# Kernel tuning notes

Hardware: AMD Instinct MI355X
Metric: run time of the kernel (lower is better)

Reference implementation:

```python
import jax, jax.numpy as jnp
import numpy as np

def setup_inputs() -> dict:
    key = jax.random.key(0)
    k1, k2 = jax.random.split(key)
    N, M, D = 4096, 4096, 1024
    set1 = jax.random.normal(k1, (N, D), dtype=jnp.float32)
    set2 = jax.random.normal(k2, (M, D), dtype=jnp.float32)
    return {"set1": set1, "set2": set2}

def _l2_dist(x, y):
    # mean over D of squared differences, computed via the expanded GEMM form
    D = x.shape[-1]
    x2 = jnp.sum(x * x, axis=-1)          # [N]
    y2 = jnp.sum(y * y, axis=-1)          # [M]
    xy = jnp.einsum('nd,md->nm', x, y)    # [N, M]
    return (x2[:, None] - 2.0 * xy + y2[None, :]) / D

def reference(set1, set2):
    dist = _l2_dist(set1, set2)                 # [N, M]
    t1 = jnp.mean(jnp.min(dist, axis=1))        # nearest set2 point per set1 point
    t2 = jnp.mean(jnp.min(dist, axis=0))        # nearest set1 point per set2 point
    return (t1 + t2) * 0.5
```

## Files before the change

### kernel.cpp

```cpp
#include <hip/hip_runtime.h>
#include <hip/hip_bf16.h>
#include <stdint.h>


#define NPTS 4096
#define MPTS 4096
#define DDIM 1024
#define SLOTB 32768

typedef __attribute__((ext_vector_type(8))) short bf16x8;
typedef __attribute__((ext_vector_type(4))) float f32x4;

__device__ __forceinline__ unsigned short f2bf(float f) {
    unsigned int u = __float_as_uint(f);
    unsigned int r = 0x7FFFu + ((u >> 16) & 1u);
    return (unsigned short)((u + r) >> 16);
}

__device__ __forceinline__ void gl_lds16(const void* g, void* l) {
    __builtin_amdgcn_global_load_lds(
        (const __attribute__((address_space(1))) unsigned int*)g,
        (__attribute__((address_space(3))) unsigned int*)l, 16, 0, 0);
}

__global__ __launch_bounds__(256) void prepass_kernel(
    const float* __restrict__ s1, const float* __restrict__ s2,
    unsigned short* __restrict__ b1, unsigned short* __restrict__ b2,
    float* __restrict__ norms, unsigned int* __restrict__ mins) {
    const int row = blockIdx.x * 4 + (threadIdx.x >> 6);
    const int lane = threadIdx.x & 63;
    const float* src;
    unsigned short* dst;
    if (row < NPTS) { src = s1 + (size_t)row * DDIM; dst = b1 + (size_t)row * DDIM; }
    else            { src = s2 + (size_t)(row - NPTS) * DDIM; dst = b2 + (size_t)(row - NPTS) * DDIM; }
    float sq = 0.f;
    #pragma unroll
    for (int i = 0; i < 4; ++i) {
        float4 v = ((const float4*)src)[lane + i * 64];
        sq += v.x * v.x + v.y * v.y + v.z * v.z + v.w * v.w;
        ushort4 o;
        o.x = f2bf(v.x); o.y = f2bf(v.y); o.z = f2bf(v.z); o.w = f2bf(v.w);
        ((ushort4*)dst)[lane + i * 64] = o;
    }
    #pragma unroll
    for (int off = 32; off; off >>= 1) sq += __shfl_down(sq, off, 64);
    if (lane == 0) { norms[row] = sq; mins[row] = 0x7f7f7f7fu; }
}


#define STAGE2(u, i0) do {                                                      \
    if ((u) < 32) {                                                             \
        const int slot_ = (u) & 3;                                              \
        const int k0_ = ((u) >> 1) * 64 + ((u) & 1) * 32;                       \
        _Pragma("unroll")                                                       \
        for (int ii_ = 0; ii_ < 2; ++ii_) {                                     \
            const int i_ = (i0) + ii_;                                          \
            const int row_ = i_ * 64 + wave * 8 + srow_l;                       \
            const unsigned short* g_ = (sc < 4)                                 \
                ? (Ab + (size_t)row_ * DDIM + k0_ + sc * 8)                     \
                : (Bb + (size_t)row_ * DDIM + k0_ + (sc - 4) * 8);              \
            gl_lds16(g_, ldsb + slot_ * SLOTB + i_ * 8192 + wave * 1024);       \
        }                                                                       \
    }                                                                           \
} while (0)

#define PHASE(slot_, FH, STAGECALL, ENDWAIT) do {                               \
    bf16x8 af_[4];                                                              \
    if ((FH) == 0) {                                                            \
        _Pragma("unroll")                                                       \
        for (int fj_ = 0; fj_ < 4; ++fj_) {                                     \
            const int col_ = wc * 64 + fj_ * 16 + r0;                           \
            bf[fj_] = *(const bf16x8*)(ldsb + (slot_) * SLOTB + col_ * 128 + chunkB); \
        }                                                                       \
    }                                                                           \
    _Pragma("unroll")                                                           \
    for (int fl_ = 0; fl_ < 4; ++fl_) {                                         \
        const int arow_ = wr * 128 + (FH) * 64 + fl_ * 16 + r0;                 \
        af_[fl_] = *(const bf16x8*)(ldsb + (slot_) * SLOTB + arow_ * 128 + chunkA); \
    }                                                                           \
    STAGECALL;                                                                  \
    __builtin_amdgcn_s_barrier();                                               \
    asm volatile("s_waitcnt lgkmcnt(0)" ::: "memory");                          \
    __builtin_amdgcn_sched_barrier(0);                                          \
    __builtin_amdgcn_s_setprio(1);                                              \
    _Pragma("unroll")                                                           \
    for (int fl_ = 0; fl_ < 4; ++fl_)                                           \
        _Pragma("unroll")                                                       \
        for (int fj_ = 0; fj_ < 4; ++fj_)                                       \
            acc[(FH) * 4 + fl_][fj_] = __builtin_amdgcn_mfma_f32_16x16x32_bf16( \
                af_[fl_], bf[fj_], acc[(FH) * 4 + fl_][fj_], 0, 0, 0);          \
    __builtin_amdgcn_s_setprio(0);                                              \
    ENDWAIT;                                                                    \
    __builtin_amdgcn_s_barrier();                                               \
    __builtin_amdgcn_sched_barrier(0);                                          \
} while (0)

__global__ __launch_bounds__(512, 2) void cham_gemm_kernel(
    const unsigned short* __restrict__ A,
    const unsigned short* __restrict__ B,
    const float* __restrict__ x2, const float* __restrict__ y2,
    unsigned int* __restrict__ rowmin, unsigned int* __restrict__ colmin) {
    __shared__ __align__(16) unsigned short lds_us[65536];
    char* ldsb = (char*)lds_us;

    const int bi = blockIdx.x & 15;
    const int bj = blockIdx.x >> 4;
    const int tid = threadIdx.x;
    const int wave = tid >> 6;
    const int lane = tid & 63;
    const int wr = wave >> 2;
    const int wc = wave & 3;
    const int r0 = lane & 15;
    const int q = lane >> 4;

    const int chunkA = ((q ^ (r0 & 7)) << 4);
    const int chunkB = (((4 + q) ^ (r0 & 7)) << 4);

    const int srow_l = lane >> 3;
    const int sc = (lane & 7) ^ srow_l;

    const unsigned short* Ab = A + (size_t)(bi * 256) * DDIM;
    const unsigned short* Bb = B + (size_t)(bj * 256) * DDIM;

    f32x4 acc[8][4];
    #pragma unroll
    for (int i = 0; i < 8; ++i)
        #pragma unroll
        for (int j = 0; j < 4; ++j)
            acc[i][j] = (f32x4){0.f, 0.f, 0.f, 0.f};

    bf16x8 bf[4];

    STAGE2(0, 0); STAGE2(0, 2);
    STAGE2(1, 0); STAGE2(1, 2);
    STAGE2(2, 0); STAGE2(2, 2);
    asm volatile("s_waitcnt vmcnt(4)" ::: "memory");
    __builtin_amdgcn_s_barrier();
    __builtin_amdgcn_sched_barrier(0);

    #pragma unroll 2
    for (int t = 0; t < 16; ++t) {
        const int s0 = (2 * t) & 3;
        const int s1 = (2 * t + 1) & 3;
        const int u0 = 2 * t + 3;
        const int u1 = 2 * t + 4;
        PHASE(s0, 0, STAGE2(u0, 0), );
        PHASE(s0, 1, STAGE2(u0, 2), );
        PHASE(s1, 0, STAGE2(u1, 0), );
        PHASE(s1, 1, STAGE2(u1, 2),
              if (t == 14) { asm volatile("s_waitcnt vmcnt(0)" ::: "memory"); }
              else if (t < 14) { asm volatile("s_waitcnt vmcnt(4)" ::: "memory"); });
    }

    const float invD = 1.0f / (float)DDIM;
    const int nb = bi * 256 + wr * 128;
    const int mb = bj * 256 + wc * 64;

    float y2v[4];
    #pragma unroll
    for (int fj = 0; fj < 4; ++fj) y2v[fj] = y2[mb + fj * 16 + r0];

    float cv[4];
    #pragma unroll
    for (int fj = 0; fj < 4; ++fj) cv[fj] = 3.0e38f;

    #pragma unroll
    for (int fi = 0; fi < 8; ++fi) {
        #pragma unroll
        for (int rg = 0; rg < 4; ++rg) {
            const int n = nb + fi * 16 + q * 4 + rg;
            const float x2v = x2[n];
            float rv = 3.0e38f;
            #pragma unroll
            for (int fj = 0; fj < 4; ++fj) {
                float d = (x2v + y2v[fj] - 2.0f * acc[fi][fj][rg]) * invD;
                rv = fminf(rv, d);
                cv[fj] = fminf(cv[fj], d);
            }
            rv = fminf(rv, __shfl_xor(rv, 1, 64));
            rv = fminf(rv, __shfl_xor(rv, 2, 64));
            rv = fminf(rv, __shfl_xor(rv, 4, 64));
            rv = fminf(rv, __shfl_xor(rv, 8, 64));
            if (r0 == 0) atomicMin(&rowmin[n], __float_as_uint(rv));
        }
    }

    #pragma unroll
    for (int fj = 0; fj < 4; ++fj) {
        float v = cv[fj];
        v = fminf(v, __shfl_xor(v, 16, 64));
        v = fminf(v, __shfl_xor(v, 32, 64));
        if (lane < 16) atomicMin(&colmin[mb + fj * 16 + lane], __float_as_uint(v));
    }
}

__global__ __launch_bounds__(1024) void finredux_kernel(
    const unsigned int* __restrict__ mins , float* __restrict__ out) {
    int t = threadIdx.x;
    float s = 0.f;
    #pragma unroll
    for (int i = 0; i < 8; ++i) s += __uint_as_float(mins[t + i * 1024]);
    #pragma unroll
    for (int off = 32; off; off >>= 1) s += __shfl_down(s, off, 64);
    __shared__ float ws_[16];
    if ((t & 63) == 0) ws_[t >> 6] = s;
    __syncthreads();
    if (t == 0) {
        float tot = 0.f;
        #pragma unroll
        for (int i = 0; i < 16; ++i) tot += ws_[i];
        out[0] = tot * (1.0f / 8192.0f);
    }
}

extern "C" void kernel_launch(void* const* d_in, const int* in_sizes, int n_in,
                              void* d_out, int out_size, void* d_ws, size_t ws_size,
                              hipStream_t stream) {
    const float* s1 = (const float*)d_in[0];
    const float* s2 = (const float*)d_in[1];
    char* ws = (char*)d_ws;

    unsigned short* b1 = (unsigned short*)ws;
    unsigned short* b2 = (unsigned short*)(ws + 8388608);
    float* norms       = (float*)(ws + 16777216);
    unsigned int* mins = (unsigned int*)(ws + 16777216 + 32768);
    float* out = (float*)d_out;

    prepass_kernel<<<2048, 256, 0, stream>>>(s1, s2, b1, b2, norms, mins);
    cham_gemm_kernel<<<256, 512, 0, stream>>>(b1, b2, norms, norms + NPTS,
                                              mins, mins + NPTS);
    finredux_kernel<<<1, 1024, 0, stream>>>(mins, out);
}
```

Baseline: 151.7 us.

## Restructure GEMM main loop into 64-wide K tiles with double-buffered quadrant phases

```diff
diff --git a/kernel.cpp b/kernel.cpp
--- a/kernel.cpp
+++ b/kernel.cpp
@@ -6,7 +6,6 @@
 #define NPTS 4096
 #define MPTS 4096
 #define DDIM 1024
-#define SLOTB 32768
 
 typedef __attribute__((ext_vector_type(8))) short bf16x8;
 typedef __attribute__((ext_vector_type(4))) float f32x4;
@@ -48,51 +47,75 @@
 }
 
 
-#define STAGE2(u, i0) do {                                                      \
-    if ((u) < 32) {                                                             \
-        const int slot_ = (u) & 3;                                              \
-        const int k0_ = ((u) >> 1) * 64 + ((u) & 1) * 32;                       \
-        _Pragma("unroll")                                                       \
-        for (int ii_ = 0; ii_ < 2; ++ii_) {                                     \
-            const int i_ = (i0) + ii_;                                          \
-            const int row_ = i_ * 64 + wave * 8 + srow_l;                       \
-            const unsigned short* g_ = (sc < 4)                                 \
-                ? (Ab + (size_t)row_ * DDIM + k0_ + sc * 8)                     \
-                : (Bb + (size_t)row_ * DDIM + k0_ + (sc - 4) * 8);              \
-            gl_lds16(g_, ldsb + slot_ * SLOTB + i_ * 8192 + wave * 1024);       \
-        }                                                                       \
-    }                                                                           \
-} while (0)
-
-#define PHASE(slot_, FH, STAGECALL, ENDWAIT) do {                               \
-    bf16x8 af_[4];                                                              \
-    if ((FH) == 0) {                                                            \
-        _Pragma("unroll")                                                       \
-        for (int fj_ = 0; fj_ < 4; ++fj_) {                                     \
-            const int col_ = wc * 64 + fj_ * 16 + r0;                           \
-            bf[fj_] = *(const bf16x8*)(ldsb + (slot_) * SLOTB + col_ * 128 + chunkB); \
-        }                                                                       \
-    }                                                                           \
+#define STAGE_H(ldsBase, gRowBase, kcol) do {                                   \
+    gl_lds16((gRowBase) + (size_t)(wave * 8 + srow) * DDIM + (kcol) + schoff,   \
+             ldsb + (ldsBase) + wave * 1024);                                   \
+    gl_lds16((gRowBase) + (size_t)(64 + wave * 8 + srow) * DDIM + (kcol) + schoff, \
+             ldsb + (ldsBase) + 8192 + wave * 1024);                            \
+} while (0)
+
+#define RD_A(CURB, aq) do {                                                     \
     _Pragma("unroll")                                                           \
     for (int fl_ = 0; fl_ < 4; ++fl_) {                                         \
-        const int arow_ = wr * 128 + (FH) * 64 + fl_ * 16 + r0;                 \
-        af_[fl_] = *(const bf16x8*)(ldsb + (slot_) * SLOTB + arow_ * 128 + chunkA); \
+        const int row_ = wr * 128 + (aq) * 64 + fl_ * 16 + r0;                  \
+        af[fl_][0] = *(const bf16x8*)(ldsb + (CURB) + row_ * 128 + ch0);        \
+        af[fl_][1] = *(const bf16x8*)(ldsb + (CURB) + row_ * 128 + ch1);        \
     }                                                                           \
-    STAGECALL;                                                                  \
+} while (0)
+
+#define RD_B(CURB, bq, dst) do {                                                \
+    _Pragma("unroll")                                                           \
+    for (int fj_ = 0; fj_ < 2; ++fj_) {                                         \
+        const int col_ = wc * 64 + (bq) * 32 + fj_ * 16 + r0;                   \
+        dst[fj_][0] = *(const bf16x8*)(ldsb + (CURB) + 32768 + col_ * 128 + ch0); \
+        dst[fj_][1] = *(const bf16x8*)(ldsb + (CURB) + 32768 + col_ * 128 + ch1); \
+    }                                                                           \
+} while (0)
+
+#define MFMA_Q(aq, bq, BF)                                                      \
+    _Pragma("unroll")                                                           \
+    for (int fl_ = 0; fl_ < 4; ++fl_) {                                         \
+        _Pragma("unroll")                                                       \
+        for (int fj_ = 0; fj_ < 2; ++fj_) {                                     \
+            acc[(aq) * 4 + fl_][(bq) * 2 + fj_] =                               \
+                __builtin_amdgcn_mfma_f32_16x16x32_bf16(af[fl_][0], BF[fj_][0], \
+                    acc[(aq) * 4 + fl_][(bq) * 2 + fj_], 0, 0, 0);              \
+            acc[(aq) * 4 + fl_][(bq) * 2 + fj_] =                               \
+                __builtin_amdgcn_mfma_f32_16x16x32_bf16(af[fl_][1], BF[fj_][1], \
+                    acc[(aq) * 4 + fl_][(bq) * 2 + fj_], 0, 0, 0);              \
+        }                                                                       \
+    }
+
+#define BARRIER_MFMA(aq, bq, BF, WAITSTMT) do {                                 \
     __builtin_amdgcn_s_barrier();                                               \
     asm volatile("s_waitcnt lgkmcnt(0)" ::: "memory");                          \
     __builtin_amdgcn_sched_barrier(0);                                          \
     __builtin_amdgcn_s_setprio(1);                                              \
-    _Pragma("unroll")                                                           \
-    for (int fl_ = 0; fl_ < 4; ++fl_)                                           \
-        _Pragma("unroll")                                                       \
-        for (int fj_ = 0; fj_ < 4; ++fj_)                                       \
-            acc[(FH) * 4 + fl_][fj_] = __builtin_amdgcn_mfma_f32_16x16x32_bf16( \
-                af_[fl_], bf[fj_], acc[(FH) * 4 + fl_][fj_], 0, 0, 0);          \
+    MFMA_Q(aq, bq, BF);                                                         \
     __builtin_amdgcn_s_setprio(0);                                              \
-    ENDWAIT;                                                                    \
+    WAITSTMT;                                                                   \
     __builtin_amdgcn_s_barrier();                                               \
-    __builtin_amdgcn_sched_barrier(0);                                          \
+} while (0)
+
+#define TILE(t, CURB, NXTB) do {                                                \
+    const int kN1_ = ((t) + 1) * 64, kN2_ = ((t) + 2) * 64;                     \
+                                                 \
+    RD_A(CURB, 0); RD_B(CURB, 0, bf0);                                          \
+    if ((t) + 1 < 16) STAGE_H((NXTB) + 49152, Bb + 128 * DDIM, kN1_);           \
+    BARRIER_MFMA(0, 0, bf0, );                                                  \
+                                                 \
+    RD_B(CURB, 1, bf1);                                                         \
+    if ((t) + 1 < 16) STAGE_H((NXTB) + 16384, Ab + 128 * DDIM, kN1_);           \
+    BARRIER_MFMA(0, 1, bf1, );                                                  \
+                                                 \
+    RD_A(CURB, 1);                                                              \
+    if ((t) + 2 < 16) STAGE_H((CURB) + 32768, Bb, kN2_);                        \
+    BARRIER_MFMA(1, 1, bf1, );                                                  \
+                                   \
+    if ((t) + 2 < 16) STAGE_H((CURB) + 0, Ab, kN2_);                            \
+    BARRIER_MFMA(1, 0, bf0,                                                     \
+        if ((t) < 14) { asm volatile("s_waitcnt vmcnt(4)" ::: "memory"); }      \
+        else if ((t) == 14) { asm volatile("s_waitcnt vmcnt(0)" ::: "memory"); });\
 } while (0)
 
 __global__ __launch_bounds__(512, 2) void cham_gemm_kernel(
@@ -100,8 +123,8 @@
     const unsigned short* __restrict__ B,
     const float* __restrict__ x2, const float* __restrict__ y2,
     unsigned int* __restrict__ rowmin, unsigned int* __restrict__ colmin) {
-    __shared__ __align__(16) unsigned short lds_us[65536];
-    char* ldsb = (char*)lds_us;
+    __shared__ __align__(16) char lds[131072];
+    char* ldsb = lds;
 
     const int bi = blockIdx.x & 15;
     const int bj = blockIdx.x >> 4;
@@ -113,11 +136,11 @@
     const int r0 = lane & 15;
     const int q = lane >> 4;
 
-    const int chunkA = ((q ^ (r0 & 7)) << 4);
-    const int chunkB = (((4 + q) ^ (r0 & 7)) << 4);
-
-    const int srow_l = lane >> 3;
-    const int sc = (lane & 7) ^ srow_l;
+    const int ch0 = ((q ^ (r0 & 7)) << 4);
+    const int ch1 = (((4 + q) ^ (r0 & 7)) << 4);
+
+    const int srow = lane >> 3;
+    const int schoff = (((lane & 7) ^ srow) * 8);
 
     const unsigned short* Ab = A + (size_t)(bi * 256) * DDIM;
     const unsigned short* Bb = B + (size_t)(bj * 256) * DDIM;
@@ -129,27 +152,21 @@
         for (int j = 0; j < 4; ++j)
             acc[i][j] = (f32x4){0.f, 0.f, 0.f, 0.f};
 
-    bf16x8 bf[4];
-
-    STAGE2(0, 0); STAGE2(0, 2);
-    STAGE2(1, 0); STAGE2(1, 2);
-    STAGE2(2, 0); STAGE2(2, 2);
+    bf16x8 af[4][2], bf0[2][2], bf1[2][2];
+
+    STAGE_H(0 + 32768, Bb, 0);
+    STAGE_H(0 + 0, Ab, 0);
+    STAGE_H(0 + 49152, Bb + 128 * DDIM, 0);
+    STAGE_H(0 + 16384, Ab + 128 * DDIM, 0);
+    STAGE_H(65536 + 32768, Bb, 64);
+    STAGE_H(65536 + 0, Ab, 64);
     asm volatile("s_waitcnt vmcnt(4)" ::: "memory");
     __builtin_amdgcn_s_barrier();
-    __builtin_amdgcn_sched_barrier(0);
-
-    #pragma unroll 2
-    for (int t = 0; t < 16; ++t) {
-        const int s0 = (2 * t) & 3;
-        const int s1 = (2 * t + 1) & 3;
-        const int u0 = 2 * t + 3;
-        const int u1 = 2 * t + 4;
-        PHASE(s0, 0, STAGE2(u0, 0), );
-        PHASE(s0, 1, STAGE2(u0, 2), );
-        PHASE(s1, 0, STAGE2(u1, 0), );
-        PHASE(s1, 1, STAGE2(u1, 2),
-              if (t == 14) { asm volatile("s_waitcnt vmcnt(0)" ::: "memory"); }
-              else if (t < 14) { asm volatile("s_waitcnt vmcnt(4)" ::: "memory"); });
+
+    for (int tt = 0; tt < 8; ++tt) {
+        const int te = 2 * tt, to = 2 * tt + 1;
+        TILE(te, 0, 65536);
+        TILE(to, 65536, 0);
     }
 
     const float invD = 1.0f / (float)DDIM;
@@ -158,7 +175,8 @@
 
     float y2v[4];
     #pragma unroll
-    for (int fj = 0; fj < 4; ++fj) y2v[fj] = y2[mb + fj * 16 + r0];
+    for (int fj = 0; fj < 4; ++fj)
+        y2v[fj] = y2[mb + (fj >> 1) * 32 + (fj & 1) * 16 + r0];
 
     float cv[4];
     #pragma unroll
@@ -190,7 +208,9 @@
         float v = cv[fj];
         v = fminf(v, __shfl_xor(v, 16, 64));
         v = fminf(v, __shfl_xor(v, 32, 64));
-        if (lane < 16) atomicMin(&colmin[mb + fj * 16 + lane], __float_as_uint(v));
+        if (lane < 16)
+            atomicMin(&colmin[mb + (fj >> 1) * 32 + (fj & 1) * 16 + lane],
+                      __float_as_uint(v));
     }
 }
 
```

Result: faster. 123.8 us (-18.4%).
